# Kernel optimization log

Measured on AMD Instinct MI355X. Metric: run time of the kernel, lower is better.

## Reference

```python
import jax, jax.numpy as jnp
import numpy as np

N_NODES = 100000
D_SRC = 128
D_DST = 128
D_OUT = 256
N_EDGES = 600000


def setup_inputs() -> dict:
    key = jax.random.key(0)
    k1, k2, k3, k4, k5 = jax.random.split(key, 5)
    x_src = jax.random.normal(k1, (N_NODES, D_SRC), dtype=jnp.float32)
    x_dst = jax.random.normal(k2, (N_NODES, D_DST), dtype=jnp.float32)
    edge_index = jax.random.randint(k3, (2, N_EDGES), 0, N_NODES, dtype=jnp.int64)
    # Linear(in_src + in_dst, out): torch stores W as [out, in]
    fan_in = D_SRC + D_DST
    bound = 1.0 / np.sqrt(fan_in)
    W = jax.random.uniform(k4, (D_OUT, fan_in), minval=-bound, maxval=bound, dtype=jnp.float32)
    b = jax.random.uniform(k5, (D_OUT,), minval=-bound, maxval=bound, dtype=jnp.float32)
    return {"x_src": x_src, "x_dst": x_dst, "edge_index": edge_index, "W": W, "b": b}


def reference(x_src, x_dst, edge_index, W, b):
    src_idx, dst_idx = edge_index[0], edge_index[1]
    n_dst = x_dst.shape[0]
    x_j = x_src[src_idx]                                  # [E, D_SRC] gather
    summed = jax.ops.segment_sum(x_j, dst_idx, num_segments=n_dst)   # [N, D_SRC]
    count = jax.ops.segment_sum(jnp.ones((src_idx.shape[0],), dtype=x_src.dtype),
                                dst_idx, num_segments=n_dst)          # [N]
    agg = summed / jnp.maximum(count, 1.0)[:, None]        # scatter-mean
    h = jnp.concatenate([x_dst, agg], axis=-1)             # [N, D_DST+D_SRC]
    return jax.nn.relu(h @ W.T + b)                        # [N, D_OUT]
```

## Files before the change

### kernel.cpp

```cpp
#include <hip/hip_runtime.h>

#define N_NODES 100000
#define D_SRC 128
#define D_OUT 256
#define K_DIM 256
#define CAP 32
#define OVF_CAP 2048

typedef __attribute__((ext_vector_type(8))) short short8;
typedef __attribute__((ext_vector_type(4))) float float4v;

__device__ inline unsigned short f2bf(float f) {
    unsigned int u = __float_as_uint(f);
    u += 0x7FFF + ((u >> 16) & 1);
    return (unsigned short)(u >> 16);
}
__device__ inline float bf_lo(unsigned int u) { return __uint_as_float(u << 16); }
__device__ inline float bf_hi(unsigned int u) { return __uint_as_float(u & 0xFFFF0000u); }

#define PREP_SRC_BLOCKS 12500
#define PREP_DST_BLOCKS 6250
#define PREP_W_BLOCKS   32
#define PREP_Z_BLOCKS   98
#define PREP_BLOCKS (PREP_SRC_BLOCKS + PREP_DST_BLOCKS + PREP_W_BLOCKS + PREP_Z_BLOCKS)

__global__ __launch_bounds__(256) void prep_kernel(
    const float* __restrict__ x_src,
    const float* __restrict__ x_dst,
    const float* __restrict__ W,
    unsigned short* __restrict__ xsb,
    unsigned short* __restrict__ xdsw,
    unsigned short* __restrict__ wsw,
    int* __restrict__ deg)
{
    int b = blockIdx.x;
    if (b < PREP_SRC_BLOCKS) {
        int i = b * 256 + threadIdx.x;
        float4 v = ((const float4*)x_src)[i];
        ushort4 o;
        o.x = f2bf(v.x); o.y = f2bf(v.y); o.z = f2bf(v.z); o.w = f2bf(v.w);
        ((ushort4*)xsb)[i] = o;
    } else if (b < PREP_SRC_BLOCKS + PREP_DST_BLOCKS) {
        int t = (b - PREP_SRC_BLOCKS) * 256 + threadIdx.x;
        int r = t >> 4;
        int g = t & 15;
        const float4* p = (const float4*)(x_dst + (size_t)r * 128 + g * 8);
        float4 v0 = p[0], v1 = p[1];
        union { unsigned short s[8]; short8 v; } pk;
        pk.s[0] = f2bf(v0.x); pk.s[1] = f2bf(v0.y);
        pk.s[2] = f2bf(v0.z); pk.s[3] = f2bf(v0.w);
        pk.s[4] = f2bf(v1.x); pk.s[5] = f2bf(v1.y);
        pk.s[6] = f2bf(v1.z); pk.s[7] = f2bf(v1.w);
        size_t gr = ((size_t)(r >> 4) * 4 + (g >> 2)) * 64 + (r & 15) + ((g & 3) << 4);
        ((short8*)xdsw)[gr] = pk.v;
    } else if (b < PREP_SRC_BLOCKS + PREP_DST_BLOCKS + PREP_W_BLOCKS) {
        int t = (b - PREP_SRC_BLOCKS - PREP_DST_BLOCKS) * 256 + threadIdx.x;
        int r = t >> 5;
        int g = t & 31;
        const float4* p = (const float4*)(W + (size_t)r * 256 + g * 8);
        float4 v0 = p[0], v1 = p[1];
        union { unsigned short s[8]; short8 v; } pk;
        pk.s[0] = f2bf(v0.x); pk.s[1] = f2bf(v0.y);
        pk.s[2] = f2bf(v0.z); pk.s[3] = f2bf(v0.w);
        pk.s[4] = f2bf(v1.x); pk.s[5] = f2bf(v1.y);
        pk.s[6] = f2bf(v1.z); pk.s[7] = f2bf(v1.w);
        size_t gr = ((size_t)(r >> 4) * 8 + (g >> 2)) * 64 + (r & 15) + ((g & 3) << 4);
        ((short8*)wsw)[gr] = pk.v;
    } else {
        int i = (b - PREP_SRC_BLOCKS - PREP_DST_BLOCKS - PREP_W_BLOCKS) * 256 + threadIdx.x;
        if (i < (N_NODES + 4) / 4)
            ((int4*)deg)[i] = make_int4(0, 0, 0, 0);
    }
}

__global__ __launch_bounds__(256) void bucket_kernel(
    const int* __restrict__ ei,
    int* __restrict__ deg,
    int* __restrict__ ovf_cnt,
    int* __restrict__ ovf,
    int* __restrict__ bucket,
    int n_edges)
{
    int e = blockIdx.x * 256 + threadIdx.x;
    if (e >= n_edges) return;
    int s = ei[e];
    int d = ei[n_edges + e];
    int pos = atomicAdd(deg + d, 1);
    if (pos < CAP) {
        bucket[(size_t)d * CAP + pos] = s;
    } else {
        int o = atomicAdd(ovf_cnt, 1);
        if (o < OVF_CAP) { ovf[2 * o] = s; ovf[2 * o + 1] = d; }
    }
}

__global__ __launch_bounds__(256) void gather_kernel(
    const unsigned short* __restrict__ xsb,
    const int*   __restrict__ deg,
    const int*   __restrict__ bucket,
    const int*   __restrict__ ovf_cnt,
    const int*   __restrict__ ovf,
    unsigned int* __restrict__ aggsw)
{
    int node = blockIdx.x * 4 + (threadIdx.x >> 6);
    if (node >= N_NODES) return;
    int lane = threadIdx.x & 63;

    int dtot = deg[node];
    int n = (dtot < CAP) ? dtot : CAP;

    int idx = bucket[(size_t)node * CAP + (lane & 31)];

    float ax = 0.f, ay = 0.f;
    for (int base = 0; base < n; base += 8) {
        unsigned int u[8];
        #pragma unroll
        for (int j = 0; j < 8; ++j) {
            if (base + j < n) {
                int s = __shfl(idx, base + j);
                u[j] = ((const unsigned int*)(xsb + (size_t)s * D_SRC))[lane];
            } else {
                u[j] = 0;
            }
        }
        #pragma unroll
        for (int j = 0; j < 8; ++j) {
            ax += bf_lo(u[j]);
            ay += bf_hi(u[j]);
        }
    }

    if (dtot > CAP) {
        int oc = *ovf_cnt;
        if (oc > OVF_CAP) oc = OVF_CAP;
        for (int o = 0; o < oc; ++o) {
            if (ovf[2 * o + 1] == node) {
                int s0 = ovf[2 * o];
                unsigned int u0 = ((const unsigned int*)(xsb + (size_t)s0 * D_SRC))[lane];
                ax += bf_lo(u0);
                ay += bf_hi(u0);
            }
        }
    }

    float inv = 1.0f / (float)((dtot > 1) ? dtot : 1);
    unsigned int packed = (unsigned int)f2bf(ax * inv)
                        | ((unsigned int)f2bf(ay * inv) << 16);
    size_t dw = ((size_t)(node >> 4) * 4 + (lane >> 4)) * 256
              + (size_t)((node & 15) + 16 * ((lane >> 2) & 3)) * 4 + (lane & 3);
    aggsw[dw] = packed;
}

__global__ __launch_bounds__(256) void mfma_gemm_kernel(
    const short8* __restrict__ xdsw,
    const short8* __restrict__ aggsw,
    const short8* __restrict__ wsw,
    const float* __restrict__ bias,
    float*       __restrict__ out)
{
    __shared__ float eps[4][16][68];

    int wave = threadIdx.x >> 6;
    int lane = threadIdx.x & 63;
    int lrow = lane & 15;
    int kq   = lane >> 4;
    int mb   = blockIdx.x;
    int m0   = mb * 64;
    int n0   = wave * 64;

    bool mok[4];
    #pragma unroll
    for (int mf = 0; mf < 4; ++mf) mok[mf] = (m0 + mf * 16) < N_NODES;

    const short8* Ax = xdsw  + (size_t)mb * 1024 + lane;
    const short8* Ag = aggsw + (size_t)mb * 1024 + lane;
    const short8* Bw = wsw   + (size_t)wave * 2048 + lane;

    float4v acc[4][4];
    #pragma unroll
    for (int i = 0; i < 4; ++i)
        #pragma unroll
        for (int j = 0; j < 4; ++j)
            acc[i][j] = (float4v){0.f, 0.f, 0.f, 0.f};

    const short8 zfrag = (short8){0,0,0,0,0,0,0,0};
    short8 a[2][4], b[2][4];

    #pragma unroll
    for (int mf = 0; mf < 4; ++mf)
        a[0][mf] = mok[mf] ? Ax[mf * 256] : zfrag;
    #pragma unroll
    for (int nf = 0; nf < 4; ++nf)
        b[0][nf] = Bw[nf * 512];

    #pragma unroll
    for (int kc = 0; kc < 8; ++kc) {
        const int cur = kc & 1, nxt = cur ^ 1;
        if (kc < 7) {
            const int k1 = kc + 1;
            const short8* A = (k1 < 4) ? Ax : Ag;
            const int kk = (k1 < 4) ? k1 : (k1 - 4);
            #pragma unroll
            for (int mf = 0; mf < 4; ++mf)
                a[nxt][mf] = mok[mf] ? A[mf * 256 + kk * 64] : zfrag;
            #pragma unroll
            for (int nf = 0; nf < 4; ++nf)
                b[nxt][nf] = Bw[nf * 512 + k1 * 64];
        }
        #pragma unroll
        for (int mf = 0; mf < 4; ++mf)
            #pragma unroll
            for (int nf = 0; nf < 4; ++nf)
                acc[mf][nf] = __builtin_amdgcn_mfma_f32_16x16x32_bf16(
                    a[cur][mf], b[cur][nf], acc[mf][nf], 0, 0, 0);
    }

    float bv[4];
    #pragma unroll
    for (int nf = 0; nf < 4; ++nf)
        bv[nf] = bias[n0 + nf * 16 + lrow];

    int srow   = lane >> 4;
    int schunk = lane & 15;

    #pragma unroll
    for (int mf = 0; mf < 4; ++mf) {
        if (!mok[mf]) continue;
        #pragma unroll
        for (int nf = 0; nf < 4; ++nf)
            #pragma unroll
            for (int r = 0; r < 4; ++r)
                eps[wave][kq * 4 + r][nf * 16 + lrow] =
                    fmaxf(acc[mf][nf][r] + bv[nf], 0.f);
        asm volatile("s_waitcnt lgkmcnt(0)" ::: "memory");
        #pragma unroll
        for (int c = 0; c < 4; ++c) {
            int row  = c * 4 + srow;
            float4v v = *(const float4v*)&eps[wave][row][schunk * 4];
            int grow = m0 + mf * 16 + row;
            __builtin_nontemporal_store(v,
                (float4v*)(out + (size_t)grow * D_OUT + n0 + schunk * 4));
        }
        asm volatile("s_waitcnt lgkmcnt(0)" ::: "memory");
    }
}

extern "C" void kernel_launch(void* const* d_in, const int* in_sizes, int n_in,
                              void* d_out, int out_size, void* d_ws, size_t ws_size,
                              hipStream_t stream) {
    const float* x_src = (const float*)d_in[0];
    const float* x_dst = (const float*)d_in[1];
    const int*   ei    = (const int*)d_in[2];
    const float* W     = (const float*)d_in[3];
    const float* bias  = (const float*)d_in[4];
    float* out = (float*)d_out;

    int n_edges = in_sizes[2] / 2;

    int* deg     = (int*)d_ws;
    int* ovf_cnt = deg + N_NODES;
    int* ovf     = ovf_cnt + 4;
    unsigned short* wsw   = (unsigned short*)(ovf + OVF_CAP * 2);
    unsigned short* aggsw = wsw + (size_t)D_OUT * K_DIM;
    unsigned short* xdsw  = aggsw + (size_t)(N_NODES / 16) * 4 * 64 * 8;

    int* bucket = (int*)d_out;
    unsigned short* xsb = (unsigned short*)(bucket + (size_t)N_NODES * CAP);

    prep_kernel<<<PREP_BLOCKS, 256, 0, stream>>>(
        x_src, x_dst, W, xsb, xdsw, wsw, deg);

    bucket_kernel<<<(n_edges + 255) / 256, 256, 0, stream>>>(
        ei, deg, ovf_cnt, ovf, bucket, n_edges);

    gather_kernel<<<(N_NODES + 3) / 4, 256, 0, stream>>>(
        xsb, deg, bucket, ovf_cnt, ovf, (unsigned int*)aggsw);

    mfma_gemm_kernel<<<(N_NODES + 63) / 64, 256, 0, stream>>>(
        (const short8*)xdsw, (const short8*)aggsw, (const short8*)wsw, bias, out);
}
```

Baseline: 318.6 us.

## Gather four nodes per wave with 16-byte loads and double-buffered issue

The gather kernel now processes four destination nodes per wave instead of one. Each 16-lane group loads a whole bf16 row with 128-bit loads, one neighbor per group, and loads are double-buffered so the next batch is issued before the current one is accumulated. Partial sums are reduced across the groups with xor shuffles and written as one 16-byte swizzled store per lane. The aim is more memory-level parallelism and wider loads in this latency-bound gather, at the cost of more registers and idle groups when degrees within a batch of four nodes differ.

```diff
diff --git a/kernel.cpp b/kernel.cpp
--- a/kernel.cpp
+++ b/kernel.cpp
@@ -9,6 +9,7 @@
 
 typedef __attribute__((ext_vector_type(8))) short short8;
 typedef __attribute__((ext_vector_type(4))) float float4v;
+typedef __attribute__((ext_vector_type(4))) unsigned int uint4v;
 
 __device__ inline unsigned short f2bf(float f) {
     unsigned int u = __float_as_uint(f);
@@ -94,6 +95,35 @@
     }
 }
 
+#define G_ISSUE(U, V, B)                                                      \
+    {                                                                         \
+        int r_ = (B) + grp;                                                   \
+        { bool v_ = r_ < n0; V[0] = v_; int s_ = __shfl(idx0, r_);            \
+          s_ = v_ ? s_ : 0;                                                   \
+          U[0] = *(const uint4v*)(xsb + (size_t)s_ * D_SRC + gcol * 8); }     \
+        { bool v_ = r_ < n1; V[1] = v_; int s_ = __shfl(idx1, r_);            \
+          s_ = v_ ? s_ : 0;                                                   \
+          U[1] = *(const uint4v*)(xsb + (size_t)s_ * D_SRC + gcol * 8); }     \
+        { bool v_ = r_ < n2; V[2] = v_; int s_ = __shfl(idx2, r_);            \
+          s_ = v_ ? s_ : 0;                                                   \
+          U[2] = *(const uint4v*)(xsb + (size_t)s_ * D_SRC + gcol * 8); }     \
+        { bool v_ = r_ < n3; V[3] = v_; int s_ = __shfl(idx3, r_);            \
+          s_ = v_ ? s_ : 0;                                                   \
+          U[3] = *(const uint4v*)(xsb + (size_t)s_ * D_SRC + gcol * 8); }     \
+    }
+
+#define G_ACC1(ACC, W)                                                       \
+    ACC[0] += bf_lo(W[0]); ACC[1] += bf_hi(W[0]);                            \
+    ACC[2] += bf_lo(W[1]); ACC[3] += bf_hi(W[1]);                            \
+    ACC[4] += bf_lo(W[2]); ACC[5] += bf_hi(W[2]);                            \
+    ACC[6] += bf_lo(W[3]); ACC[7] += bf_hi(W[3]);
+
+#define G_ACCUM(U, V)                                                        \
+    if (V[0]) { G_ACC1(acc0, U[0]) }                                         \
+    if (V[1]) { G_ACC1(acc1, U[1]) }                                         \
+    if (V[2]) { G_ACC1(acc2, U[2]) }                                         \
+    if (V[3]) { G_ACC1(acc3, U[3]) }
+
 __global__ __launch_bounds__(256) void gather_kernel(
     const unsigned short* __restrict__ xsb,
     const int*   __restrict__ deg,
@@ -102,53 +132,99 @@
     const int*   __restrict__ ovf,
     unsigned int* __restrict__ aggsw)
 {
-    int node = blockIdx.x * 4 + (threadIdx.x >> 6);
-    if (node >= N_NODES) return;
+    int wid  = threadIdx.x >> 6;
     int lane = threadIdx.x & 63;
-
-    int dtot = deg[node];
-    int n = (dtot < CAP) ? dtot : CAP;
-
-    int idx = bucket[(size_t)node * CAP + (lane & 31)];
-
-    float ax = 0.f, ay = 0.f;
-    for (int base = 0; base < n; base += 8) {
-        unsigned int u[8];
-        #pragma unroll
-        for (int j = 0; j < 8; ++j) {
-            if (base + j < n) {
-                int s = __shfl(idx, base + j);
-                u[j] = ((const unsigned int*)(xsb + (size_t)s * D_SRC))[lane];
-            } else {
-                u[j] = 0;
-            }
+    int nbase = (blockIdx.x * 4 + wid) * 4;
+    if (nbase >= N_NODES) return;
+    int grp  = lane >> 4;
+    int gcol = lane & 15;
+
+    int dl  = deg[nbase + (lane & 3)];
+    int dt0 = __shfl(dl, 0), dt1 = __shfl(dl, 1);
+    int dt2 = __shfl(dl, 2), dt3 = __shfl(dl, 3);
+    int n0 = min(dt0, CAP), n1 = min(dt1, CAP);
+    int n2 = min(dt2, CAP), n3 = min(dt3, CAP);
+
+    int idx0 = bucket[(size_t)(nbase + 0) * CAP + (lane & 31)];
+    int idx1 = bucket[(size_t)(nbase + 1) * CAP + (lane & 31)];
+    int idx2 = bucket[(size_t)(nbase + 2) * CAP + (lane & 31)];
+    int idx3 = bucket[(size_t)(nbase + 3) * CAP + (lane & 31)];
+
+    float acc0[8] = {0,0,0,0,0,0,0,0}, acc1[8] = {0,0,0,0,0,0,0,0};
+    float acc2[8] = {0,0,0,0,0,0,0,0}, acc3[8] = {0,0,0,0,0,0,0,0};
+
+    int maxn = max(max(n0, n1), max(n2, n3));
+
+    uint4v uA[4], uB[4];
+    bool   vA[4], vB[4];
+    if (maxn > 0) {
+        G_ISSUE(uA, vA, 0)
+        int b = 0;
+        while (true) {
+            if (b + 4 < maxn) { G_ISSUE(uB, vB, b + 4) }
+            G_ACCUM(uA, vA)
+            b += 4;
+            if (b >= maxn) break;
+            if (b + 4 < maxn) { G_ISSUE(uA, vA, b + 4) }
+            G_ACCUM(uB, vB)
+            b += 4;
+            if (b >= maxn) break;
         }
-        #pragma unroll
-        for (int j = 0; j < 8; ++j) {
-            ax += bf_lo(u[j]);
-            ay += bf_hi(u[j]);
-        }
-    }
-
-    if (dtot > CAP) {
+    }
+
+    if ((dt0 > CAP) | (dt1 > CAP) | (dt2 > CAP) | (dt3 > CAP)) {
         int oc = *ovf_cnt;
         if (oc > OVF_CAP) oc = OVF_CAP;
         for (int o = 0; o < oc; ++o) {
-            if (ovf[2 * o + 1] == node) {
+            int od  = ovf[2 * o + 1];
+            int rel = od - nbase;
+            if (rel >= 0 && rel < 4) {
                 int s0 = ovf[2 * o];
-                unsigned int u0 = ((const unsigned int*)(xsb + (size_t)s0 * D_SRC))[lane];
-                ax += bf_lo(u0);
-                ay += bf_hi(u0);
+                uint4v w = *(const uint4v*)(xsb + (size_t)s0 * D_SRC + gcol * 8);
+                if (grp == 0) {
+                    if      (rel == 0) { G_ACC1(acc0, w) }
+                    else if (rel == 1) { G_ACC1(acc1, w) }
+                    else if (rel == 2) { G_ACC1(acc2, w) }
+                    else               { G_ACC1(acc3, w) }
+                }
             }
         }
     }
 
-    float inv = 1.0f / (float)((dtot > 1) ? dtot : 1);
-    unsigned int packed = (unsigned int)f2bf(ax * inv)
-                        | ((unsigned int)f2bf(ay * inv) << 16);
-    size_t dw = ((size_t)(node >> 4) * 4 + (lane >> 4)) * 256
-              + (size_t)((node & 15) + 16 * ((lane >> 2) & 3)) * 4 + (lane & 3);
-    aggsw[dw] = packed;
+    #pragma unroll
+    for (int k = 0; k < 8; ++k) {
+        acc0[k] += __shfl_xor(acc0[k], 16); acc0[k] += __shfl_xor(acc0[k], 32);
+        acc1[k] += __shfl_xor(acc1[k], 16); acc1[k] += __shfl_xor(acc1[k], 32);
+        acc2[k] += __shfl_xor(acc2[k], 16); acc2[k] += __shfl_xor(acc2[k], 32);
+        acc3[k] += __shfl_xor(acc3[k], 16); acc3[k] += __shfl_xor(acc3[k], 32);
+    }
+
+    int dsel = dt0;
+    dsel = (grp == 1) ? dt1 : dsel;
+    dsel = (grp == 2) ? dt2 : dsel;
+    dsel = (grp == 3) ? dt3 : dsel;
+    float inv = 1.0f / (float)((dsel > 1) ? dsel : 1);
+
+    float sum[8];
+    #pragma unroll
+    for (int k = 0; k < 8; ++k) {
+        float v = acc0[k];
+        v = (grp == 1) ? acc1[k] : v;
+        v = (grp == 2) ? acc2[k] : v;
+        v = (grp == 3) ? acc3[k] : v;
+        sum[k] = v * inv;
+    }
+
+    uint4v o;
+    o[0] = (unsigned)f2bf(sum[0]) | ((unsigned)f2bf(sum[1]) << 16);
+    o[1] = (unsigned)f2bf(sum[2]) | ((unsigned)f2bf(sum[3]) << 16);
+    o[2] = (unsigned)f2bf(sum[4]) | ((unsigned)f2bf(sum[5]) << 16);
+    o[3] = (unsigned)f2bf(sum[6]) | ((unsigned)f2bf(sum[7]) << 16);
+
+    int node = nbase + grp;
+    size_t gr = ((size_t)(node >> 4) * 4 + (gcol >> 2)) * 64
+              + (node & 15) + ((gcol & 3) << 4);
+    ((uint4v*)aggsw)[gr] = o;
 }
 
 __global__ __launch_bounds__(256) void mfma_gemm_kernel(
@@ -273,7 +349,7 @@
     bucket_kernel<<<(n_edges + 255) / 256, 256, 0, stream>>>(
         ei, deg, ovf_cnt, ovf, bucket, n_edges);
 
-    gather_kernel<<<(N_NODES + 3) / 4, 256, 0, stream>>>(
+    gather_kernel<<<(N_NODES + 15) / 16, 256, 0, stream>>>(
         xsb, deg, bucket, ovf_cnt, ovf, (unsigned int*)aggsw);
 
     mfma_gemm_kernel<<<(N_NODES + 63) / 64, 256, 0, stream>>>(
```

After: 289.8 us. 9.0% less time.
